# Optimization experiments

Hardware: AMD Instinct MI355X
Metric: run time of the kernel (lower is better)

The kernel has to match this reference:

```python
import jax, jax.numpy as jnp
import numpy as np

N = 100000      # nodes
E = 1600000     # edges (avg degree 16)
DIN, DH, DOUT = 128, 128, 64


def setup_inputs() -> dict:
    key = jax.random.key(0)
    k0, k1, k2, k3 = jax.random.split(key, 4)
    x = jax.random.normal(k0, (N, DIN), jnp.float32)
    edge_index = jax.random.randint(k1, (2, E), 0, N, dtype=jnp.int64)
    W1 = jax.random.normal(k2, (DIN, DH), jnp.float32) / np.sqrt(DIN).astype(np.float32)
    b1 = jnp.zeros((DH,), jnp.float32)
    W2 = jax.random.normal(k3, (DH, DOUT), jnp.float32) / np.sqrt(DH).astype(np.float32)
    b2 = jnp.zeros((DOUT,), jnp.float32)
    return {"x": x, "edge_index": edge_index, "W1": W1, "b1": b1, "W2": W2, "b2": b2}


def reference(x, edge_index, W1, b1, W2, b2):
    n = x.shape[0]
    # PyG GCNConv: add self-loops, symmetric normalization deg^-1/2 A_hat deg^-1/2
    loops = jnp.arange(n, dtype=edge_index.dtype)
    src = jnp.concatenate([edge_index[0], loops])  # message sources
    dst = jnp.concatenate([edge_index[1], loops])  # aggregation targets
    deg = jax.ops.segment_sum(jnp.ones(src.shape, x.dtype), dst, num_segments=n)
    dinv = jnp.where(deg > 0, jax.lax.rsqrt(deg), 0.0)
    norm = dinv[src] * dinv[dst]                    # [E+N]

    def gcn_conv(h, W, b):
        h = h @ W                                   # dense transform first (PyG order)
        msg = h[src] * norm[:, None]                # gather + scale
        return jax.ops.segment_sum(msg, dst, num_segments=n) + b

    h = jax.nn.relu(gcn_conv(x, W1, b1))
    # F.dropout is identity in eval mode (self.training == False)
    return gcn_conv(h, W2, b2)
```

## Files before the change

### kernel.cpp

```cpp
#include <hip/hip_runtime.h>

#define DIN 128
#define DH  128
#define DOUT 64

typedef __attribute__((ext_vector_type(8))) short bf16x8;
typedef __attribute__((ext_vector_type(4))) float f32x4;


__device__ inline unsigned bf16rne(float f) {
    unsigned u = __float_as_uint(f);
    return (u + 0x7fffu + ((u >> 16) & 1u)) >> 16;
}

__device__ inline void acc8(float* a, uint4 v) {
    a[0] += __uint_as_float(v.x << 16); a[1] += __uint_as_float(v.x & 0xffff0000u);
    a[2] += __uint_as_float(v.y << 16); a[3] += __uint_as_float(v.y & 0xffff0000u);
    a[4] += __uint_as_float(v.z << 16); a[5] += __uint_as_float(v.z & 0xffff0000u);
    a[6] += __uint_as_float(v.w << 16); a[7] += __uint_as_float(v.w & 0xffff0000u);
}


__global__ void k_count_rank(const int* __restrict__ dst, int* __restrict__ cnt,
                             int* __restrict__ rank, int E, int pad) {
    int e = blockIdx.x * 256 + threadIdx.x;
    if (e < E) rank[e] = atomicAdd(&cnt[dst[e] * pad], 1);
}

__global__ void k_dinv(const int* __restrict__ cnt, float* __restrict__ dinv, int n, int pad) {
    int i = blockIdx.x * 256 + threadIdx.x;
    if (i < n) dinv[i] = rsqrtf((float)(cnt[i * pad] + 1));
}

__global__ void k_scan_partial(const int* __restrict__ cnt, int* __restrict__ excl,
                               int* __restrict__ bsum, int n, int pad) {
    __shared__ int sd[256];
    int t = threadIdx.x;
    int base = blockIdx.x * 1024 + t * 4;
    int v0 = (base + 0 < n) ? cnt[(base + 0) * pad] : 0;
    int v1 = (base + 1 < n) ? cnt[(base + 1) * pad] : 0;
    int v2 = (base + 2 < n) ? cnt[(base + 2) * pad] : 0;
    int v3 = (base + 3 < n) ? cnt[(base + 3) * pad] : 0;
    int s = v0 + v1 + v2 + v3;
    sd[t] = s;
    __syncthreads();
    for (int off = 1; off < 256; off <<= 1) {
        int x = (t >= off) ? sd[t - off] : 0;
        __syncthreads();
        sd[t] += x;
        __syncthreads();
    }
    int incl = sd[t];
    if (t == 255) bsum[blockIdx.x] = incl;
    int run = incl - s;
    if (base + 0 < n) excl[base + 0] = run;  run += v0;
    if (base + 1 < n) excl[base + 1] = run;  run += v1;
    if (base + 2 < n) excl[base + 2] = run;  run += v2;
    if (base + 3 < n) excl[base + 3] = run;
}

__global__ void k_scan_bsum(int* __restrict__ bsum, int nb) {
    __shared__ int sd[256];
    int t = threadIdx.x;
    int v = (t < nb) ? bsum[t] : 0;
    sd[t] = v;
    __syncthreads();
    for (int off = 1; off < 256; off <<= 1) {
        int x = (t >= off) ? sd[t - off] : 0;
        __syncthreads();
        sd[t] += x;
        __syncthreads();
    }
    if (t < nb) bsum[t] = sd[t] - v;
}

__global__ void k_finalize(int* __restrict__ rowstart, const int* __restrict__ bsum,
                           int n, int E) {
    int i = blockIdx.x * 256 + threadIdx.x;
    if (i < n) rowstart[i] += bsum[i >> 10];
    if (i == 0) rowstart[n] = E;
}


__global__ void k_wsplit_frag(const float* __restrict__ W, unsigned short* __restrict__ Wf_hi,
                              unsigned short* __restrict__ Wf_lo, int N) {
    int idx = blockIdx.x * 256 + threadIdx.x;
    if (idx >= N * 128) return;
    int f = idx >> 9;
    int r = idx & 511;
    int lane = r >> 3;
    int j = r & 7;
    int t = f >> 2;
    int ks = f & 3;
    int n = t * 16 + (lane & 15);
    int k = ks * 32 + (lane >> 4) * 8 + j;
    float v = W[(size_t)k * N + n];
    unsigned h = bf16rne(v);
    float hf = __uint_as_float(h << 16);
    unsigned l = bf16rne(v - hf);
    Wf_hi[idx] = (unsigned short)h;
    Wf_lo[idx] = (unsigned short)l;
}


template <int NCOLS>
__device__ __forceinline__ void gemm_f32A_body(
        int bid, const float* __restrict__ A,
        const unsigned short* __restrict__ Bh, const unsigned short* __restrict__ Bl,
        const float* __restrict__ dinv, unsigned short* __restrict__ S, int M) {
    constexpr int NT = NCOLS / 16;
    int wave = threadIdx.x >> 6;
    int lane = threadIdx.x & 63;
    int row0 = bid * 64 + wave * 16;
    int arow = row0 + (lane & 15);
    if (arow >= M) arow = M - 1;
    const float* ap = A + (size_t)arow * 128 + (lane >> 4) * 8;
    const unsigned short* bhp = Bh + lane * 8;
    const unsigned short* blp = Bl + lane * 8;

    float4 a0 = *(const float4*)(ap);
    float4 a1 = *(const float4*)(ap + 4);

    f32x4 acc[NT];
    #pragma unroll
    for (int t = 0; t < NT; t++) acc[t] = (f32x4){0.f, 0.f, 0.f, 0.f};

    #pragma unroll
    for (int ks = 0; ks < 4; ks++) {
        float4 n0, n1;
        if (ks < 3) {
            n0 = *(const float4*)(ap + (ks + 1) * 32);
            n1 = *(const float4*)(ap + (ks + 1) * 32 + 4);
        }
        float a8[8] = {a0.x, a0.y, a0.z, a0.w, a1.x, a1.y, a1.z, a1.w};
        bf16x8 ahi, alo;
        #pragma unroll
        for (int j = 0; j < 8; j++) {
            unsigned h = bf16rne(a8[j]);
            float hf = __uint_as_float(h << 16);
            ahi[j] = (short)h;
            alo[j] = (short)bf16rne(a8[j] - hf);
        }
        #pragma unroll
        for (int t = 0; t < NT; t++) {
            bf16x8 bh = *(const bf16x8*)(bhp + (size_t)(t * 4 + ks) * 512);
            bf16x8 bl = *(const bf16x8*)(blp + (size_t)(t * 4 + ks) * 512);
            acc[t] = __builtin_amdgcn_mfma_f32_16x16x32_bf16(ahi, bh, acc[t], 0, 0, 0);
            acc[t] = __builtin_amdgcn_mfma_f32_16x16x32_bf16(ahi, bl, acc[t], 0, 0, 0);
            acc[t] = __builtin_amdgcn_mfma_f32_16x16x32_bf16(alo, bh, acc[t], 0, 0, 0);
        }
        a0 = n0; a1 = n1;
    }

    int srow0 = row0 + (lane >> 4) * 4;
    int bcol = lane & 15;
    #pragma unroll
    for (int r = 0; r < 4; r++) {
        int row = srow0 + r;
        float dv = (row < M) ? dinv[row] : 0.f;
        #pragma unroll
        for (int t = 0; t < NT; t++) {
            unsigned o = bf16rne(dv * acc[t][r]);
            unsigned p = (unsigned)__shfl_xor((int)o, 1);
            if ((lane & 1) == 0 && row < M)
                *(unsigned*)(S + (size_t)row * NCOLS + t * 16 + bcol) = o | (p << 16);
        }
    }
}

template <int NCOLS>
__global__ __launch_bounds__(256, 4) void k_fill_gemm(
        const int* __restrict__ src, const int* __restrict__ dst,
        const int* __restrict__ rank, const int* __restrict__ rowstart,
        int* __restrict__ adj, int E, int gemm_blocks,
        const float* __restrict__ A, const unsigned short* __restrict__ Bh,
        const unsigned short* __restrict__ Bl, const float* __restrict__ dinv,
        unsigned short* __restrict__ S, int M) {
    int bid = blockIdx.x;
    if (bid < gemm_blocks) {
        gemm_f32A_body<NCOLS>(bid, A, Bh, Bl, dinv, S, M);
    } else {
        int e = (bid - gemm_blocks) * 256 + threadIdx.x;
        if (e < E) adj[rowstart[dst[e]] + rank[e]] = src[e];
    }
}

template <int NCOLS>
__global__ __launch_bounds__(256, 4) void k_gemm_bf16A(
        const unsigned short* __restrict__ A,
        const unsigned short* __restrict__ Bh, const unsigned short* __restrict__ Bl,
        const float* __restrict__ dinv, unsigned short* __restrict__ S, int M) {
    constexpr int NT = NCOLS / 16;
    int wave = threadIdx.x >> 6;
    int lane = threadIdx.x & 63;
    int row0 = blockIdx.x * 64 + wave * 16;
    int arow = row0 + (lane & 15);
    if (arow >= M) arow = M - 1;
    const unsigned short* ap = A + (size_t)arow * 128 + (lane >> 4) * 8;
    const unsigned short* bhp = Bh + lane * 8;
    const unsigned short* blp = Bl + lane * 8;

    bf16x8 a = *(const bf16x8*)(ap);

    f32x4 acc[NT];
    #pragma unroll
    for (int t = 0; t < NT; t++) acc[t] = (f32x4){0.f, 0.f, 0.f, 0.f};

    #pragma unroll
    for (int ks = 0; ks < 4; ks++) {
        bf16x8 anext;
        if (ks < 3) anext = *(const bf16x8*)(ap + (ks + 1) * 32);
        #pragma unroll
        for (int t = 0; t < NT; t++) {
            bf16x8 bh = *(const bf16x8*)(bhp + (size_t)(t * 4 + ks) * 512);
            bf16x8 bl = *(const bf16x8*)(blp + (size_t)(t * 4 + ks) * 512);
            acc[t] = __builtin_amdgcn_mfma_f32_16x16x32_bf16(a, bh, acc[t], 0, 0, 0);
            acc[t] = __builtin_amdgcn_mfma_f32_16x16x32_bf16(a, bl, acc[t], 0, 0, 0);
        }
        a = anext;
    }

    int srow0 = row0 + (lane >> 4) * 4;
    int bcol = lane & 15;
    #pragma unroll
    for (int r = 0; r < 4; r++) {
        int row = srow0 + r;
        float dv = (row < M) ? dinv[row] : 0.f;
        #pragma unroll
        for (int t = 0; t < NT; t++) {
            unsigned o = bf16rne(dv * acc[t][r]);
            unsigned p = (unsigned)__shfl_xor((int)o, 1);
            if ((lane & 1) == 0 && row < M)
                *(unsigned*)(S + (size_t)row * NCOLS + t * 16 + bcol) = o | (p << 16);
        }
    }
}


__global__ void k_agg128(const unsigned short* __restrict__ S, const int* __restrict__ rowstart,
                         const int* __restrict__ adj, const float* __restrict__ dinv,
                         const float* __restrict__ bias, unsigned short* __restrict__ out, int n) {
    int wave = threadIdx.x >> 6;
    int lane = threadIdx.x & 63;
    int node = blockIdx.x * 4 + wave;
    if (node >= n) return;
    int start = rowstart[node];
    int end   = rowstart[node + 1];
    int g  = lane >> 4;
    int fo = lane & 15;

    const uint4* S4 = (const uint4*)S;
    float a0[8] = {}, a1[8] = {};

    while (start < end) {
        int cnt = end - start;
        if (cnt > 64) cnt = 64;
        int nb = adj[start + (lane < cnt ? lane : cnt - 1)];
        int t = 0;
        for (; t + 16 <= cnt; t += 16) {
            int jA = __shfl(nb, t + 0  + g);
            int jB = __shfl(nb, t + 4  + g);
            int jC = __shfl(nb, t + 8  + g);
            int jD = __shfl(nb, t + 12 + g);
            uint4 mA = S4[(size_t)jA * 16 + fo];
            uint4 mB = S4[(size_t)jB * 16 + fo];
            uint4 mC = S4[(size_t)jC * 16 + fo];
            uint4 mD = S4[(size_t)jD * 16 + fo];
            acc8(a0, mA); acc8(a1, mB); acc8(a0, mC); acc8(a1, mD);
        }
        for (; t + 4 <= cnt; t += 4) {
            int j = __shfl(nb, t + g);
            uint4 m = S4[(size_t)j * 16 + fo];
            acc8(a0, m);
        }
        if (t < cnt) {
            int i1 = t + g;
            int j = __shfl(nb, i1 < cnt ? i1 : cnt - 1);
            uint4 m = S4[(size_t)j * 16 + fo];
            if (i1 < cnt) acc8(a1, m);
        }
        start += 64;
    }

    float acc[8];
    #pragma unroll
    for (int i = 0; i < 8; i++) {
        float v = a0[i] + a1[i];
        v += __shfl_xor(v, 16);
        v += __shfl_xor(v, 32);
        acc[i] = v;
    }

    uint4 selfu = ((const uint4*)S)[(size_t)node * 16 + fo];
    float self[8] = {};
    acc8(self, selfu);
    float dv = dinv[node];
    float4 bb0 = ((const float4*)bias)[fo * 2 + 0];
    float4 bb1 = ((const float4*)bias)[fo * 2 + 1];
    float o[8];
    o[0] = dv * (acc[0] + self[0]) + bb0.x;
    o[1] = dv * (acc[1] + self[1]) + bb0.y;
    o[2] = dv * (acc[2] + self[2]) + bb0.z;
    o[3] = dv * (acc[3] + self[3]) + bb0.w;
    o[4] = dv * (acc[4] + self[4]) + bb1.x;
    o[5] = dv * (acc[5] + self[5]) + bb1.y;
    o[6] = dv * (acc[6] + self[6]) + bb1.z;
    o[7] = dv * (acc[7] + self[7]) + bb1.w;
    #pragma unroll
    for (int i = 0; i < 8; i++) o[i] = fmaxf(o[i], 0.f);
    if (g == 0) {
        uint4 w;
        w.x = bf16rne(o[0]) | (bf16rne(o[1]) << 16);
        w.y = bf16rne(o[2]) | (bf16rne(o[3]) << 16);
        w.z = bf16rne(o[4]) | (bf16rne(o[5]) << 16);
        w.w = bf16rne(o[6]) | (bf16rne(o[7]) << 16);
        ((uint4*)out)[(size_t)node * 16 + fo] = w;
    }
}

__global__ void k_agg64(const unsigned short* __restrict__ S, const int* __restrict__ rowstart,
                        const int* __restrict__ adj, const float* __restrict__ dinv,
                        const float* __restrict__ bias, float* __restrict__ out, int n) {
    int wave = threadIdx.x >> 6;
    int lane = threadIdx.x & 63;
    int node = blockIdx.x * 4 + wave;
    if (node >= n) return;
    int start = rowstart[node];
    int end   = rowstart[node + 1];
    int g  = lane >> 3;
    int fo = lane & 7;

    const uint4* S4 = (const uint4*)S;
    float a0[8] = {}, a1[8] = {};

    while (start < end) {
        int cnt = end - start;
        if (cnt > 64) cnt = 64;
        int nb = adj[start + (lane < cnt ? lane : cnt - 1)];
        int t = 0;
        for (; t + 32 <= cnt; t += 32) {
            int jA = __shfl(nb, t + 0  + g);
            int jB = __shfl(nb, t + 8  + g);
            int jC = __shfl(nb, t + 16 + g);
            int jD = __shfl(nb, t + 24 + g);
            uint4 mA = S4[(size_t)jA * 8 + fo];
            uint4 mB = S4[(size_t)jB * 8 + fo];
            uint4 mC = S4[(size_t)jC * 8 + fo];
            uint4 mD = S4[(size_t)jD * 8 + fo];
            acc8(a0, mA); acc8(a1, mB); acc8(a0, mC); acc8(a1, mD);
        }
        for (; t + 8 <= cnt; t += 8) {
            int j = __shfl(nb, t + g);
            uint4 m = S4[(size_t)j * 8 + fo];
            acc8(a0, m);
        }
        if (t < cnt) {
            int i1 = t + g;
            int j = __shfl(nb, i1 < cnt ? i1 : cnt - 1);
            uint4 m = S4[(size_t)j * 8 + fo];
            if (i1 < cnt) acc8(a1, m);
        }
        start += 64;
    }

    float acc[8];
    #pragma unroll
    for (int i = 0; i < 8; i++) {
        float v = a0[i] + a1[i];
        v += __shfl_xor(v, 8);
        v += __shfl_xor(v, 16);
        v += __shfl_xor(v, 32);
        acc[i] = v;
    }

    uint4 selfu = ((const uint4*)S)[(size_t)node * 8 + fo];
    float self[8] = {};
    acc8(self, selfu);
    float dv = dinv[node];
    float4 bb0 = ((const float4*)bias)[fo * 2 + 0];
    float4 bb1 = ((const float4*)bias)[fo * 2 + 1];
    float o[8];
    o[0] = dv * (acc[0] + self[0]) + bb0.x;
    o[1] = dv * (acc[1] + self[1]) + bb0.y;
    o[2] = dv * (acc[2] + self[2]) + bb0.z;
    o[3] = dv * (acc[3] + self[3]) + bb0.w;
    o[4] = dv * (acc[4] + self[4]) + bb1.x;
    o[5] = dv * (acc[5] + self[5]) + bb1.y;
    o[6] = dv * (acc[6] + self[6]) + bb1.z;
    o[7] = dv * (acc[7] + self[7]) + bb1.w;
    if (g == 0) {
        float4* op = (float4*)(out + (size_t)node * 64 + fo * 8);
        op[0] = make_float4(o[0], o[1], o[2], o[3]);
        op[1] = make_float4(o[4], o[5], o[6], o[7]);
    }
}


extern "C" void kernel_launch(void* const* d_in, const int* in_sizes, int n_in,
                              void* d_out, int out_size, void* d_ws, size_t ws_size,
                              hipStream_t stream) {
    const float* x  = (const float*)d_in[0];
    const int*   ei = (const int*)d_in[1];
    const float* W1 = (const float*)d_in[2];
    const float* b1 = (const float*)d_in[3];
    const float* W2 = (const float*)d_in[4];
    const float* b2 = (const float*)d_in[5];
    float* out = (float*)d_out;

    int N = in_sizes[0] / DIN;
    int E = in_sizes[1] / 2;
    const int* esrc = ei;
    const int* edst = ei + E;

    size_t fixed = (size_t)N * 128 * 2
                 + (size_t)N * 128 * 2
                 + (size_t)N * 4
                 + (size_t)(N + 1) * 4
                 + (size_t)E * 4 * 2
                 + (128 + 64) * 128 * 2 * 2
                 + 1024 * 4 + 16 * 256;
    int PAD = (fixed + (size_t)N * 16 * 4 <= ws_size) ? 16 : 1;

    char* wsb = (char*)d_ws;
    size_t off = 0;
    auto alloc = [&](size_t bytes) {
        void* p = wsb + off;
        off = (off + bytes + 255) & ~(size_t)255;
        return p;
    };
    unsigned short* S  = (unsigned short*)alloc((size_t)N * 128 * 2);
    unsigned short* H1 = (unsigned short*)alloc((size_t)N * 128 * 2);
    float* dinv     = (float*)alloc((size_t)N * 4);
    int*   rowstart = (int*)alloc((size_t)(N + 1) * 4);
    int*   adj      = (int*)alloc((size_t)E * 4);
    int*   rank     = (int*)alloc((size_t)E * 4);
    unsigned short* wf1h = (unsigned short*)alloc(128 * 128 * 2);
    unsigned short* wf1l = (unsigned short*)alloc(128 * 128 * 2);
    unsigned short* wf2h = (unsigned short*)alloc(64 * 128 * 2);
    unsigned short* wf2l = (unsigned short*)alloc(64 * 128 * 2);
    int*   cnt      = (int*)alloc((size_t)N * PAD * 4);
    int*   bsum     = (int*)alloc(1024 * 4);

    int eb = (E + 255) / 256;
    int nb = (N + 255) / 256;
    int sb = (N + 1023) / 1024;

    k_wsplit_frag<<<(128 * 128) / 256, 256, 0, stream>>>(W1, wf1h, wf1l, 128);
    k_wsplit_frag<<<(64 * 128) / 256, 256, 0, stream>>>(W2, wf2h, wf2l, 64);

    hipMemsetAsync(cnt, 0, (size_t)N * PAD * 4, stream);
    k_count_rank<<<eb, 256, 0, stream>>>(edst, cnt, rank, E, PAD);
    k_dinv<<<nb, 256, 0, stream>>>(cnt, dinv, N, PAD);
    k_scan_partial<<<sb, 256, 0, stream>>>(cnt, rowstart, bsum, N, PAD);
    k_scan_bsum<<<1, 256, 0, stream>>>(bsum, sb);
    k_finalize<<<nb, 256, 0, stream>>>(rowstart, bsum, N, E);

    int gb = (N + 63) / 64;
    int ab = (N + 3) / 4;

    k_fill_gemm<128><<<gb + eb, 256, 0, stream>>>(esrc, edst, rank, rowstart, adj, E, gb,
                                                  x, wf1h, wf1l, dinv, S, N);
    k_agg128<<<ab, 256, 0, stream>>>(S, rowstart, adj, dinv, b1, H1, N);

    k_gemm_bf16A<64><<<gb, 256, 0, stream>>>(H1, wf2h, wf2l, dinv, S, N);
    k_agg64<<<ab, 256, 0, stream>>>(S, rowstart, adj, dinv, b2, out, N);
}
```

Before: 250.5 us.

## Overlap first GEMM with degree counting, fuse prep and dinv, defer scaling

One prep kernel now does the weight bf16 splitting and the zeroing of the count buffer, replacing two launches and a memset. The layer-1 GEMM no longer needs dinv, so it runs in the same interleaved kernel as the atomic degree counting. The dinv scaling of S moves into a later pass that is interleaved with the CSR fill, and dinv is computed inside the scan kernel. This removes launches and serial dependencies, but adds an extra read-modify-write pass over S and a second bf16 rounding of S.

Measured after the change: 301.8 us. 1.2x slower.

```diff
diff --git a/kernel.cpp b/kernel.cpp
--- a/kernel.cpp
+++ b/kernel.cpp
@@ -21,71 +21,10 @@
 }
 
 
-__global__ void k_count_rank(const int* __restrict__ dst, int* __restrict__ cnt,
-                             int* __restrict__ rank, int E, int pad) {
-    int e = blockIdx.x * 256 + threadIdx.x;
-    if (e < E) rank[e] = atomicAdd(&cnt[dst[e] * pad], 1);
-}
-
-__global__ void k_dinv(const int* __restrict__ cnt, float* __restrict__ dinv, int n, int pad) {
-    int i = blockIdx.x * 256 + threadIdx.x;
-    if (i < n) dinv[i] = rsqrtf((float)(cnt[i * pad] + 1));
-}
-
-__global__ void k_scan_partial(const int* __restrict__ cnt, int* __restrict__ excl,
-                               int* __restrict__ bsum, int n, int pad) {
-    __shared__ int sd[256];
-    int t = threadIdx.x;
-    int base = blockIdx.x * 1024 + t * 4;
-    int v0 = (base + 0 < n) ? cnt[(base + 0) * pad] : 0;
-    int v1 = (base + 1 < n) ? cnt[(base + 1) * pad] : 0;
-    int v2 = (base + 2 < n) ? cnt[(base + 2) * pad] : 0;
-    int v3 = (base + 3 < n) ? cnt[(base + 3) * pad] : 0;
-    int s = v0 + v1 + v2 + v3;
-    sd[t] = s;
-    __syncthreads();
-    for (int off = 1; off < 256; off <<= 1) {
-        int x = (t >= off) ? sd[t - off] : 0;
-        __syncthreads();
-        sd[t] += x;
-        __syncthreads();
-    }
-    int incl = sd[t];
-    if (t == 255) bsum[blockIdx.x] = incl;
-    int run = incl - s;
-    if (base + 0 < n) excl[base + 0] = run;  run += v0;
-    if (base + 1 < n) excl[base + 1] = run;  run += v1;
-    if (base + 2 < n) excl[base + 2] = run;  run += v2;
-    if (base + 3 < n) excl[base + 3] = run;
-}
-
-__global__ void k_scan_bsum(int* __restrict__ bsum, int nb) {
-    __shared__ int sd[256];
-    int t = threadIdx.x;
-    int v = (t < nb) ? bsum[t] : 0;
-    sd[t] = v;
-    __syncthreads();
-    for (int off = 1; off < 256; off <<= 1) {
-        int x = (t >= off) ? sd[t - off] : 0;
-        __syncthreads();
-        sd[t] += x;
-        __syncthreads();
-    }
-    if (t < nb) bsum[t] = sd[t] - v;
-}
-
-__global__ void k_finalize(int* __restrict__ rowstart, const int* __restrict__ bsum,
-                           int n, int E) {
-    int i = blockIdx.x * 256 + threadIdx.x;
-    if (i < n) rowstart[i] += bsum[i >> 10];
-    if (i == 0) rowstart[n] = E;
-}
-
-
-__global__ void k_wsplit_frag(const float* __restrict__ W, unsigned short* __restrict__ Wf_hi,
-                              unsigned short* __restrict__ Wf_lo, int N) {
-    int idx = blockIdx.x * 256 + threadIdx.x;
-    if (idx >= N * 128) return;
+__device__ __forceinline__ void wsplit_body(const float* __restrict__ W,
+                                            unsigned short* __restrict__ Wh,
+                                            unsigned short* __restrict__ Wl,
+                                            int N, int idx) {
     int f = idx >> 9;
     int r = idx & 511;
     int lane = r >> 3;
@@ -98,8 +37,24 @@
     unsigned h = bf16rne(v);
     float hf = __uint_as_float(h << 16);
     unsigned l = bf16rne(v - hf);
-    Wf_hi[idx] = (unsigned short)h;
-    Wf_lo[idx] = (unsigned short)l;
+    Wh[idx] = (unsigned short)h;
+    Wl[idx] = (unsigned short)l;
+}
+
+__global__ void k_prep(const float* __restrict__ W1, unsigned short* __restrict__ wf1h,
+                       unsigned short* __restrict__ wf1l,
+                       const float* __restrict__ W2, unsigned short* __restrict__ wf2h,
+                       unsigned short* __restrict__ wf2l,
+                       uint4* __restrict__ cntz, int nz4, int w1b, int w2b) {
+    int bid = blockIdx.x;
+    if (bid < w1b) {
+        wsplit_body(W1, wf1h, wf1l, 128, bid * 256 + threadIdx.x);
+    } else if (bid < w1b + w2b) {
+        wsplit_body(W2, wf2h, wf2l, 64, (bid - w1b) * 256 + threadIdx.x);
+    } else {
+        int i = (bid - w1b - w2b) * 256 + threadIdx.x;
+        if (i < nz4) cntz[i] = make_uint4(0u, 0u, 0u, 0u);
+    }
 }
 
 
@@ -107,7 +62,7 @@
 __device__ __forceinline__ void gemm_f32A_body(
         int bid, const float* __restrict__ A,
         const unsigned short* __restrict__ Bh, const unsigned short* __restrict__ Bl,
-        const float* __restrict__ dinv, unsigned short* __restrict__ S, int M) {
+        unsigned short* __restrict__ S, int M) {
     constexpr int NT = NCOLS / 16;
     int wave = threadIdx.x >> 6;
     int lane = threadIdx.x & 63;
@@ -157,10 +112,9 @@
     #pragma unroll
     for (int r = 0; r < 4; r++) {
         int row = srow0 + r;
-        float dv = (row < M) ? dinv[row] : 0.f;
         #pragma unroll
         for (int t = 0; t < NT; t++) {
-            unsigned o = bf16rne(dv * acc[t][r]);
+            unsigned o = bf16rne(acc[t][r]);
             unsigned p = (unsigned)__shfl_xor((int)o, 1);
             if ((lane & 1) == 0 && row < M)
                 *(unsigned*)(S + (size_t)row * NCOLS + t * 16 + bcol) = o | (p << 16);
@@ -169,21 +123,106 @@
 }
 
 template <int NCOLS>
-__global__ __launch_bounds__(256, 4) void k_fill_gemm(
-        const int* __restrict__ src, const int* __restrict__ dst,
-        const int* __restrict__ rank, const int* __restrict__ rowstart,
-        int* __restrict__ adj, int E, int gemm_blocks,
+__global__ __launch_bounds__(256, 4) void k_cg(
         const float* __restrict__ A, const unsigned short* __restrict__ Bh,
-        const unsigned short* __restrict__ Bl, const float* __restrict__ dinv,
-        unsigned short* __restrict__ S, int M) {
+        const unsigned short* __restrict__ Bl, unsigned short* __restrict__ S,
+        int M, int gb, int R,
+        const int* __restrict__ dst, int* __restrict__ cnt, int* __restrict__ rank,
+        int E, int pad) {
     int bid = blockIdx.x;
-    if (bid < gemm_blocks) {
-        gemm_f32A_body<NCOLS>(bid, A, Bh, Bl, dinv, S, M);
+    int q = bid / R, r = bid % R;
+    if (r == 0 && q < gb) {
+        gemm_f32A_body<NCOLS>(q, A, Bh, Bl, S, M);
     } else {
-        int e = (bid - gemm_blocks) * 256 + threadIdx.x;
+        int ntag = (q < gb) ? (q + (r ? 1 : 0)) : gb;
+        int e = (bid - ntag) * 256 + threadIdx.x;
+        if (e < E) rank[e] = atomicAdd(&cnt[dst[e] * pad], 1);
+    }
+}
+
+
+__global__ void k_scan_partial(const int* __restrict__ cnt, int* __restrict__ excl,
+                               int* __restrict__ bsum, float* __restrict__ dinv,
+                               int n, int pad) {
+    __shared__ int sd[256];
+    int t = threadIdx.x;
+    int base = blockIdx.x * 1024 + t * 4;
+    int v0 = (base + 0 < n) ? cnt[(base + 0) * pad] : 0;
+    int v1 = (base + 1 < n) ? cnt[(base + 1) * pad] : 0;
+    int v2 = (base + 2 < n) ? cnt[(base + 2) * pad] : 0;
+    int v3 = (base + 3 < n) ? cnt[(base + 3) * pad] : 0;
+    if (base + 0 < n) dinv[base + 0] = rsqrtf((float)(v0 + 1));
+    if (base + 1 < n) dinv[base + 1] = rsqrtf((float)(v1 + 1));
+    if (base + 2 < n) dinv[base + 2] = rsqrtf((float)(v2 + 1));
+    if (base + 3 < n) dinv[base + 3] = rsqrtf((float)(v3 + 1));
+    int s = v0 + v1 + v2 + v3;
+    sd[t] = s;
+    __syncthreads();
+    for (int off = 1; off < 256; off <<= 1) {
+        int x = (t >= off) ? sd[t - off] : 0;
+        __syncthreads();
+        sd[t] += x;
+        __syncthreads();
+    }
+    int incl = sd[t];
+    if (t == 255) bsum[blockIdx.x] = incl;
+    int run = incl - s;
+    if (base + 0 < n) excl[base + 0] = run;  run += v0;
+    if (base + 1 < n) excl[base + 1] = run;  run += v1;
+    if (base + 2 < n) excl[base + 2] = run;  run += v2;
+    if (base + 3 < n) excl[base + 3] = run;
+}
+
+__global__ void k_scan_bsum(int* __restrict__ bsum, int nb) {
+    __shared__ int sd[256];
+    int t = threadIdx.x;
+    int v = (t < nb) ? bsum[t] : 0;
+    sd[t] = v;
+    __syncthreads();
+    for (int off = 1; off < 256; off <<= 1) {
+        int x = (t >= off) ? sd[t - off] : 0;
+        __syncthreads();
+        sd[t] += x;
+        __syncthreads();
+    }
+    if (t < nb) bsum[t] = sd[t] - v;
+}
+
+__global__ void k_finalize(int* __restrict__ rowstart, const int* __restrict__ bsum,
+                           int n, int E) {
+    int i = blockIdx.x * 256 + threadIdx.x;
+    if (i < n) rowstart[i] += bsum[i >> 10];
+    if (i == 0) rowstart[n] = E;
+}
+
+__global__ void k_fill_scale(const int* __restrict__ src, const int* __restrict__ dst,
+                             const int* __restrict__ rank, const int* __restrict__ rowstart,
+                             int* __restrict__ adj, int E, int fillb, int R,
+                             uint4* __restrict__ S4, const float* __restrict__ dinv, int su4) {
+    int bid = blockIdx.x;
+    int q = bid / R, r = bid % R;
+    if (r == 0 && q < fillb) {
+        int e = q * 256 + threadIdx.x;
         if (e < E) adj[rowstart[dst[e]] + rank[e]] = src[e];
-    }
-}
+    } else {
+        int ntag = (q < fillb) ? (q + (r ? 1 : 0)) : fillb;
+        int i = (bid - ntag) * 256 + threadIdx.x;
+        if (i < su4) {
+            float dv = dinv[i >> 4];
+            uint4 v = S4[i];
+            v.x = bf16rne(__uint_as_float(v.x << 16) * dv) |
+                  (bf16rne(__uint_as_float(v.x & 0xffff0000u) * dv) << 16);
+            v.y = bf16rne(__uint_as_float(v.y << 16) * dv) |
+                  (bf16rne(__uint_as_float(v.y & 0xffff0000u) * dv) << 16);
+            v.z = bf16rne(__uint_as_float(v.z << 16) * dv) |
+                  (bf16rne(__uint_as_float(v.z & 0xffff0000u) * dv) << 16);
+            v.w = bf16rne(__uint_as_float(v.w << 16) * dv) |
+                  (bf16rne(__uint_as_float(v.w & 0xffff0000u) * dv) << 16);
+            S4[i] = v;
+        }
+    }
+}
+
 
 template <int NCOLS>
 __global__ __launch_bounds__(256, 4) void k_gemm_bf16A(
@@ -444,22 +483,30 @@
     int eb = (E + 255) / 256;
     int nb = (N + 255) / 256;
     int sb = (N + 1023) / 1024;
-
-    k_wsplit_frag<<<(128 * 128) / 256, 256, 0, stream>>>(W1, wf1h, wf1l, 128);
-    k_wsplit_frag<<<(64 * 128) / 256, 256, 0, stream>>>(W2, wf2h, wf2l, 64);
-
-    hipMemsetAsync(cnt, 0, (size_t)N * PAD * 4, stream);
-    k_count_rank<<<eb, 256, 0, stream>>>(edst, cnt, rank, E, PAD);
-    k_dinv<<<nb, 256, 0, stream>>>(cnt, dinv, N, PAD);
-    k_scan_partial<<<sb, 256, 0, stream>>>(cnt, rowstart, bsum, N, PAD);
+    int gb = (N + 63) / 64;
+    int ab = (N + 3) / 4;
+
+    int w1b = (128 * 128) / 256;
+    int w2b = (64 * 128) / 256;
+    int nz4 = (N * PAD) / 4;
+    int zb = (nz4 + 255) / 256;
+    k_prep<<<w1b + w2b + zb, 256, 0, stream>>>(W1, wf1h, wf1l, W2, wf2h, wf2l,
+                                               (uint4*)cnt, nz4, w1b, w2b);
+
+    int Rcg = (gb + eb) / gb; if (Rcg < 1) Rcg = 1;
+    k_cg<128><<<gb + eb, 256, 0, stream>>>(x, wf1h, wf1l, S, N, gb, Rcg,
+                                           edst, cnt, rank, E, PAD);
+
+    k_scan_partial<<<sb, 256, 0, stream>>>(cnt, rowstart, bsum, dinv, N, PAD);
     k_scan_bsum<<<1, 256, 0, stream>>>(bsum, sb);
     k_finalize<<<nb, 256, 0, stream>>>(rowstart, bsum, N, E);
 
-    int gb = (N + 63) / 64;
-    int ab = (N + 3) / 4;
-
-    k_fill_gemm<128><<<gb + eb, 256, 0, stream>>>(esrc, edst, rank, rowstart, adj, E, gb,
-                                                  x, wf1h, wf1l, dinv, S, N);
+    int su4 = N * 16;
+    int scb = (su4 + 255) / 256;
+    int Rfs = (eb + scb) / eb; if (Rfs < 1) Rfs = 1;
+    k_fill_scale<<<eb + scb, 256, 0, stream>>>(esrc, edst, rank, rowstart, adj, E, eb, Rfs,
+                                               (uint4*)S, dinv, su4);
+
     k_agg128<<<ab, 256, 0, stream>>>(S, rowstart, adj, dinv, b1, H1, N);
 
     k_gemm_bf16A<64><<<gb, 256, 0, stream>>>(H1, wf2h, wf2l, dinv, S, N);
```
